# Kernel optimization log

Hardware: AMD Instinct MI355X
Metric: run time of the kernel (lower is better)

The kernel has to match this reference:

```python
import jax, jax.numpy as jnp
import numpy as np

K, D, S, H = 8, 2, 1, 12  # kernel_size, dilation, stride, h_size


def setup_inputs() -> dict:
    key = jax.random.key(0)
    k1, k2 = jax.random.split(key)
    x = jax.random.normal(k1, (32, 2048, 64), dtype=jnp.float32)
    A = jax.random.normal(k2, (64, H, H), dtype=jnp.float32) * 0.1
    return {"x": x, "A": A}


def reference(x, A):
    B, T, C = x.shape
    pad = (K + (K - 1) * (D - 1) - 1) // 2  # = 7
    # replicate padding along time
    xp = jnp.pad(x, ((0, 0), (pad, pad), (0, 0)), mode='edge')  # (B, Tp, C)
    Tp = xp.shape[1]
    seg = (Tp - (K - 1) * D - 1) // S + 1
    # dilated unfold: gather overlapping windows along time
    idx = jnp.arange(seg)[:, None] * S + jnp.arange(K)[None, :] * D  # (seg, K)
    win = xp[:, idx, :]                       # (B, seg, K, C)
    w = win.reshape(B * seg, K, C)            # (N, K, C)
    # path increments within each window
    dx = w[:, 1:, :] - w[:, :-1, :]           # (N, K-1, C)
    # skew-symmetric (so(n)) parametrisation of the Lie-algebra map
    Ask = A - jnp.swapaxes(A, -1, -2)         # (C, H, H)
    M = jnp.einsum('nkc,chw->nkhw', dx, Ask)  # (N, K-1, H, H)
    # matrix exponential of each increment's Lie-algebra element
    E = jax.vmap(jax.scipy.linalg.expm)(M.reshape(-1, H, H)).reshape(M.shape)
    # sequential development: z_{t+1} = z_t @ exp(M_t), z_0 = I
    z0 = jnp.broadcast_to(jnp.eye(H, dtype=x.dtype), (B * seg, H, H))

    def step(z, e):
        return jnp.matmul(z, e), None

    zT, _ = jax.lax.scan(step, z0, jnp.swapaxes(E, 0, 1))  # scan over K-1 steps
    dev = zT.reshape(B, seg, H * H)
    sp = w[:, 0, :].reshape(B, seg, C)        # start point of each partition
    return jnp.concatenate([dev, sp], axis=-1)  # (B, seg, H*H + C)
```

## Files before the change

### kernel.cpp

```cpp
#include <hip/hip_runtime.h>

#define B_ 32
#define T_ 2048
#define C_ 64
#define NP_ 2060
#define MSTRIDE 144
#define LSTRIDE 148
#define W3_ 96
#define NE3_ 110

typedef short short8_t __attribute__((ext_vector_type(8)));
typedef float f32x4 __attribute__((ext_vector_type(4)));

__device__ __forceinline__ unsigned short f2bf(float f) {
  unsigned u = __float_as_uint(f);
  return (unsigned short)((u + 0x7FFFu + ((u >> 16) & 1u)) >> 16);
}
__device__ __forceinline__ float bf2f(unsigned short s) {
  return __uint_as_float(((unsigned)s) << 16);
}

__global__ __launch_bounds__(256) void k1_mfma(const float* __restrict__ x,
                                               const float* __restrict__ A,
                                               float* __restrict__ M) {
  __shared__ unsigned int askw[9216];
  const int b = blockIdx.y;
  const int p0 = blockIdx.x * 64;
  const int tid = threadIdx.x;
  const float sc = 1.0f / 32.0f;

  for (int P = tid; P < 4608; P += 256) {
    const int j2 = P & 3;
    const int col = (P >> 2) & 15;
    const int koct = (P >> 6) & 3;
    const int rest = P >> 8;
    const int tile = rest % 9;
    const int ks = rest / 9;
    const int e = tile * 16 + col;
    const int h = e / 12, w = e - h * 12;
    const int c0 = ks * 32 + koct * 8 + j2 * 2;
    const float v0 = (A[c0 * 144 + e] - A[c0 * 144 + w * 12 + h]) * sc;
    const float v1 = (A[(c0 + 1) * 144 + e] - A[(c0 + 1) * 144 + w * 12 + h]) * sc;
    const unsigned short h0 = f2bf(v0), h1 = f2bf(v1);
    const unsigned short l0 = f2bf(v0 - bf2f(h0)), l1 = f2bf(v1 - bf2f(h1));
    const int widx = (((ks * 9 + tile) * 4 + koct) * 16 + col) * 4 + j2;
    askw[widx] = ((unsigned)h1 << 16) | h0;
    askw[4608 + widx] = ((unsigned)l1 << 16) | l0;
  }
  __syncthreads();

  const int wv = tid >> 6;
  const int lane = tid & 63;
  const int mrow = lane & 15;
  const int koct = lane >> 4;
  const int p = p0 + wv * 16 + mrow;
  const int i1 = min(max(p - 7, 0), T_ - 1);
  const int i2 = min(max(p - 5, 0), T_ - 1);
  const float* xb = x + (size_t)b * T_ * C_;

  short8_t ah[2], al[2];
#pragma unroll
  for (int ks = 0; ks < 2; ++ks) {
    const int c0 = ks * 32 + koct * 8;
    const float4 u1a = *(const float4*)(xb + (size_t)i1 * C_ + c0);
    const float4 u1b = *(const float4*)(xb + (size_t)i1 * C_ + c0 + 4);
    const float4 u2a = *(const float4*)(xb + (size_t)i2 * C_ + c0);
    const float4 u2b = *(const float4*)(xb + (size_t)i2 * C_ + c0 + 4);
    float d[8];
    d[0] = u2a.x - u1a.x; d[1] = u2a.y - u1a.y;
    d[2] = u2a.z - u1a.z; d[3] = u2a.w - u1a.w;
    d[4] = u2b.x - u1b.x; d[5] = u2b.y - u1b.y;
    d[6] = u2b.z - u1b.z; d[7] = u2b.w - u1b.w;
#pragma unroll
    for (int j = 0; j < 8; ++j) {
      const unsigned short hs = f2bf(d[j]);
      ah[ks][j] = (short)hs;
      al[ks][j] = (short)f2bf(d[j] - bf2f(hs));
    }
  }

  float* Mb = M + (size_t)b * NP_ * MSTRIDE;
  const int dcol = lane & 15;
  const int pbase = p0 + wv * 16 + (lane >> 4) * 4;
  const char* lds = (const char*)askw;
#pragma unroll
  for (int tile = 0; tile < 9; ++tile) {
    f32x4 acc = {0.f, 0.f, 0.f, 0.f};
#pragma unroll
    for (int ks = 0; ks < 2; ++ks) {
      const int fb = (((ks * 9 + tile) * 4 + koct) * 16 + dcol) * 16;
      const short8_t bh = *(const short8_t*)(lds + fb);
      const short8_t bl = *(const short8_t*)(lds + 18432 + fb);
      acc = __builtin_amdgcn_mfma_f32_16x16x32_bf16(ah[ks], bh, acc, 0, 0, 0);
      acc = __builtin_amdgcn_mfma_f32_16x16x32_bf16(ah[ks], bl, acc, 0, 0, 0);
      acc = __builtin_amdgcn_mfma_f32_16x16x32_bf16(al[ks], bh, acc, 0, 0, 0);
    }
#pragma unroll
    for (int reg = 0; reg < 4; ++reg) {
      const int pr = pbase + reg;
      if (pr < NP_) Mb[(size_t)pr * MSTRIDE + tile * 16 + dcol] = acc[reg];
    }
  }
}

template <int Q>
__device__ __forceinline__ float qb(float v) {
  return __int_as_float(
      __builtin_amdgcn_mov_dpp(__float_as_int(v), Q * 0x55, 0xf, 0xf, true));
}

template <bool ACC>
__device__ __forceinline__ void qmm_t(const float a[3][12], const float b[3][12],
                                      float c[3][12]) {
  if (!ACC) {
#pragma unroll
    for (int i = 0; i < 3; ++i)
#pragma unroll
      for (int j = 0; j < 12; ++j) c[i][j] = 0.f;
  }
#define QMM_K(OWNER, E)                                                  \
  {                                                                      \
    float bk[12];                                                        \
    _Pragma("unroll")                                                    \
    for (int j = 0; j < 12; ++j) bk[j] = qb<OWNER>(b[E][j]);             \
    _Pragma("unroll")                                                    \
    for (int i = 0; i < 3; ++i) {                                        \
      const float av = a[i][3 * OWNER + E];                              \
      _Pragma("unroll")                                                  \
      for (int j = 0; j < 12; ++j) c[i][j] = fmaf(av, bk[j], c[i][j]);   \
    }                                                                    \
  }
  QMM_K(0, 0) QMM_K(0, 1) QMM_K(0, 2)
  QMM_K(1, 0) QMM_K(1, 1) QMM_K(1, 2)
  QMM_K(2, 0) QMM_K(2, 1) QMM_K(2, 2)
  QMM_K(3, 0) QMM_K(3, 1) QMM_K(3, 2)
#undef QMM_K
}
__device__ __forceinline__ void qmm(const float a[3][12], const float b[3][12],
                                    float c[3][12]) { qmm_t<false>(a, b, c); }
__device__ __forceinline__ void qmma(const float a[3][12], const float b[3][12],
                                     float c[3][12]) { qmm_t<true>(a, b, c); }

__global__ __launch_bounds__(256) void k2_expm(float* __restrict__ M) {
  const int gq = (blockIdx.x * 256 + threadIdx.x) >> 2;
  const int r = threadIdx.x & 3;
  float* gp = M + (size_t)gq * MSTRIDE + 36 * r;

  float a[3][12], t2[3][12], t3[3][12];
#pragma unroll
  for (int i = 0; i < 3; ++i)
#pragma unroll
    for (int q4 = 0; q4 < 3; ++q4) {
      float4 v = *(const float4*)(gp + i * 12 + q4 * 4);
      a[i][q4 * 4 + 0] = v.x;
      a[i][q4 * 4 + 1] = v.y;
      a[i][q4 * 4 + 2] = v.z;
      a[i][q4 * 4 + 3] = v.w;
    }

  qmm(a, a, t2);
  qmm(t2, a, t3);
#pragma unroll
  for (int i = 0; i < 3; ++i)
#pragma unroll
    for (int j = 0; j < 12; ++j) {
      const float av = a[i][j], t2v = t2[i][j], t3v = t3[i][j];
      t2[i][j] = av + t2v * 0.5f + t3v * (1.0f / 6.0f) +
                 ((j == 3 * r + i) ? 1.0f : 0.0f);
      a[i][j] = av * (1.0f / 24.0f) + t2v * (1.0f / 120.0f) +
                t3v * (1.0f / 720.0f);
    }
  qmma(t3, a, t2);

  qmm(t2, t2, t3);
  qmm(t3, t3, t2);
  qmm(t2, t2, t3);
  qmm(t3, t3, t2);
  qmm(t2, t2, t3);

#pragma unroll
  for (int i = 0; i < 3; ++i)
#pragma unroll
    for (int q4 = 0; q4 < 3; ++q4)
      *(float4*)(gp + i * 12 + q4 * 4) =
          make_float4(t3[i][q4 * 4 + 0], t3[i][q4 * 4 + 1],
                      t3[i][q4 * 4 + 2], t3[i][q4 * 4 + 3]);
}

__global__ __launch_bounds__(256) void k3_pair(const float* __restrict__ E,
                                               const float* __restrict__ x,
                                               float* __restrict__ out) {
  __shared__ float eb[NE3_][LSTRIDE];
  const int b = blockIdx.y;
  const int t0 = blockIdx.x * W3_;
  const float* src = E + (size_t)b * NP_ * MSTRIDE;
  for (int i = threadIdx.x; i < NE3_ * 36; i += 256) {
    const int m = i / 36, q = i - m * 36;
    const int p = min(t0 + m, NP_ - 1);
    *(float4*)(&eb[m][q * 4]) = *(const float4*)(src + (size_t)p * MSTRIDE + q * 4);
  }
  __syncthreads();

  const int r = threadIdx.x & 3;
  const int pr = threadIdx.x >> 2;
  if (pr >= 48) return;
  const int par = pr & 1, jj = pr >> 1;
  const int tloc = 4 * jj + par;
  const int t1 = t0 + tloc;

#define LOADB(DST, IDX)                                                  \
  {                                                                      \
    _Pragma("unroll")                                                    \
    for (int i = 0; i < 3; ++i) {                                        \
      const float* ep = &eb[(IDX)][(3 * r + i) * 12];                    \
      float4 v0 = *(const float4*)(ep + 0);                              \
      float4 v1 = *(const float4*)(ep + 4);                              \
      float4 v2 = *(const float4*)(ep + 8);                              \
      DST[i][0] = v0.x; DST[i][1] = v0.y; DST[i][2]  = v0.z; DST[i][3]  = v0.w; \
      DST[i][4] = v1.x; DST[i][5] = v1.y; DST[i][6]  = v1.z; DST[i][7]  = v1.w; \
      DST[i][8] = v2.x; DST[i][9] = v2.y; DST[i][10] = v2.z; DST[i][11] = v2.w; \
    }                                                                    \
  }

#define STOREZ(SRCZ, TW)                                                 \
  {                                                                      \
    const size_t obase = ((size_t)b * T_ + (TW)) * 208;                  \
    _Pragma("unroll")                                                    \
    for (int i = 0; i < 3; ++i) {                                        \
      const int row = 3 * r + i;                                         \
      *(float4*)(out + obase + row * 12 + 0) =                           \
          make_float4(SRCZ[i][0], SRCZ[i][1], SRCZ[i][2],  SRCZ[i][3]);  \
      *(float4*)(out + obase + row * 12 + 4) =                           \
          make_float4(SRCZ[i][4], SRCZ[i][5], SRCZ[i][6],  SRCZ[i][7]);  \
      *(float4*)(out + obase + row * 12 + 8) =                           \
          make_float4(SRCZ[i][8], SRCZ[i][9], SRCZ[i][10], SRCZ[i][11]); \
    }                                                                    \
    const int xi = min(max((TW) - 7, 0), T_ - 1);                        \
    const float* xr = x + ((size_t)b * T_ + xi) * C_ + 16 * r;           \
    _Pragma("unroll")                                                    \
    for (int qd = 0; qd < 4; ++qd) {                                     \
      *(float4*)(out + obase + 144 + 16 * r + qd * 4) =                  \
          *(const float4*)(xr + qd * 4);                                 \
    }                                                                    \
  }

  float rr[3][12], cc[3][12], bb[3][12];
  LOADB(rr, tloc + 2);
  LOADB(bb, tloc + 4);  qmm(rr, bb, cc);
  LOADB(bb, tloc + 6);  qmm(cc, bb, rr);
  LOADB(bb, tloc + 8);  qmm(rr, bb, cc);
  LOADB(bb, tloc + 10); qmm(cc, bb, rr);
  LOADB(bb, tloc + 12); qmm(rr, bb, cc);

  LOADB(bb, tloc);      qmm(bb, cc, rr);
  if (t1 < T_) STOREZ(rr, t1);
  LOADB(bb, tloc + 14); qmm(cc, bb, rr);
  if (t1 + 2 < T_) STOREZ(rr, t1 + 2);
#undef LOADB
#undef STOREZ
}

extern "C" void kernel_launch(void* const* d_in, const int* in_sizes, int n_in,
                              void* d_out, int out_size, void* d_ws, size_t ws_size,
                              hipStream_t stream) {
  (void)in_sizes; (void)n_in; (void)out_size;
  const float* x = (const float*)d_in[0];
  const float* A = (const float*)d_in[1];
  float* out = (float*)d_out;
  float* M = (float*)d_ws;

  const size_t need = (size_t)B_ * NP_ * MSTRIDE * sizeof(float);
  if (ws_size < need) return;

  k1_mfma<<<dim3(33, B_), 256, 0, stream>>>(x, A, M);
  k2_expm<<<dim3((B_ * NP_ * 4) / 256), 256, 0, stream>>>(M);
  k3_pair<<<dim3((T_ + W3_ - 1) / W3_, B_), 256, 0, stream>>>(M, x, out);
}
```

Baseline: 122.0 us.

## Drop one expm squaring step and read k3 matrices straight from global memory

The expm scaling factor is reduced from 1/32 to 1/16, so the squaring phase needs one fewer 12x12 matrix multiply per element. This trades a little Taylor accuracy for less compute in the exponential kernel. The pair-product kernel no longer stages E matrices through shared memory. Each thread now loads directly from global/L2 with all 256 threads active over a 128-step tile, removing the shared-memory fill, the barrier and the idle threads, at the cost of redundant global reads.

```diff
diff --git a/kernel.cpp b/kernel.cpp
--- a/kernel.cpp
+++ b/kernel.cpp
@@ -5,9 +5,6 @@
 #define C_ 64
 #define NP_ 2060
 #define MSTRIDE 144
-#define LSTRIDE 148
-#define W3_ 96
-#define NE3_ 110
 
 typedef short short8_t __attribute__((ext_vector_type(8)));
 typedef float f32x4 __attribute__((ext_vector_type(4)));
@@ -27,7 +24,7 @@
   const int b = blockIdx.y;
   const int p0 = blockIdx.x * 64;
   const int tid = threadIdx.x;
-  const float sc = 1.0f / 32.0f;
+  const float sc = 1.0f / 16.0f;
 
   for (int P = tid; P < 4608; P += 256) {
     const int j2 = P & 3;
@@ -176,46 +173,37 @@
   qmm(t3, t3, t2);
   qmm(t2, t2, t3);
   qmm(t3, t3, t2);
-  qmm(t2, t2, t3);
 
 #pragma unroll
   for (int i = 0; i < 3; ++i)
 #pragma unroll
     for (int q4 = 0; q4 < 3; ++q4)
       *(float4*)(gp + i * 12 + q4 * 4) =
-          make_float4(t3[i][q4 * 4 + 0], t3[i][q4 * 4 + 1],
-                      t3[i][q4 * 4 + 2], t3[i][q4 * 4 + 3]);
+          make_float4(t2[i][q4 * 4 + 0], t2[i][q4 * 4 + 1],
+                      t2[i][q4 * 4 + 2], t2[i][q4 * 4 + 3]);
 }
 
 __global__ __launch_bounds__(256) void k3_pair(const float* __restrict__ E,
                                                const float* __restrict__ x,
                                                float* __restrict__ out) {
-  __shared__ float eb[NE3_][LSTRIDE];
   const int b = blockIdx.y;
-  const int t0 = blockIdx.x * W3_;
-  const float* src = E + (size_t)b * NP_ * MSTRIDE;
-  for (int i = threadIdx.x; i < NE3_ * 36; i += 256) {
-    const int m = i / 36, q = i - m * 36;
-    const int p = min(t0 + m, NP_ - 1);
-    *(float4*)(&eb[m][q * 4]) = *(const float4*)(src + (size_t)p * MSTRIDE + q * 4);
-  }
-  __syncthreads();
+  const int t0 = blockIdx.x * 128;
+  const float* Eb = E + (size_t)b * NP_ * MSTRIDE;
 
   const int r = threadIdx.x & 3;
-  const int pr = threadIdx.x >> 2;
-  if (pr >= 48) return;
-  const int par = pr & 1, jj = pr >> 1;
+  const int q = threadIdx.x >> 2;
+  const int par = q & 1, jj = q >> 1;
   const int tloc = 4 * jj + par;
   const int t1 = t0 + tloc;
 
-#define LOADB(DST, IDX)                                                  \
+#define LOADB_G(DST, P)                                                  \
   {                                                                      \
+    const float* ep = Eb + (size_t)(P) * MSTRIDE + (3 * r) * 12;         \
     _Pragma("unroll")                                                    \
     for (int i = 0; i < 3; ++i) {                                        \
-      const float* ep = &eb[(IDX)][(3 * r + i) * 12];                    \
-      float4 v0 = *(const float4*)(ep + 0);                              \
-      float4 v1 = *(const float4*)(ep + 4);                              \
-      float4 v2 = *(const float4*)(ep + 8);                              \
+      float4 v0 = *(const float4*)(ep + i * 12 + 0);                     \
+      float4 v1 = *(const float4*)(ep + i * 12 + 4);                     \
+      float4 v2 = *(const float4*)(ep + i * 12 + 8);                     \
       DST[i][0] = v0.x; DST[i][1] = v0.y; DST[i][2]  = v0.z; DST[i][3]  = v0.w; \
       DST[i][4] = v1.x; DST[i][5] = v1.y; DST[i][6]  = v1.z; DST[i][7]  = v1.w; \
       DST[i][8] = v2.x; DST[i][9] = v2.y; DST[i][10] = v2.z; DST[i][11] = v2.w; \
@@ -245,18 +233,18 @@
   }
 
   float rr[3][12], cc[3][12], bb[3][12];
-  LOADB(rr, tloc + 2);
-  LOADB(bb, tloc + 4);  qmm(rr, bb, cc);
-  LOADB(bb, tloc + 6);  qmm(cc, bb, rr);
-  LOADB(bb, tloc + 8);  qmm(rr, bb, cc);
-  LOADB(bb, tloc + 10); qmm(cc, bb, rr);
-  LOADB(bb, tloc + 12); qmm(rr, bb, cc);
-
-  LOADB(bb, tloc);      qmm(bb, cc, rr);
-  if (t1 < T_) STOREZ(rr, t1);
-  LOADB(bb, tloc + 14); qmm(cc, bb, rr);
-  if (t1 + 2 < T_) STOREZ(rr, t1 + 2);
-#undef LOADB
+  LOADB_G(rr, t1 + 2);
+  LOADB_G(bb, t1 + 4);  qmm(rr, bb, cc);
+  LOADB_G(bb, t1 + 6);  qmm(cc, bb, rr);
+  LOADB_G(bb, t1 + 8);  qmm(rr, bb, cc);
+  LOADB_G(bb, t1 + 10); qmm(cc, bb, rr);
+  LOADB_G(bb, t1 + 12); qmm(rr, bb, cc);
+
+  LOADB_G(bb, t1);      qmm(bb, cc, rr);
+  STOREZ(rr, t1);
+  LOADB_G(bb, t1 + 14); qmm(cc, bb, rr);
+  STOREZ(rr, t1 + 2);
+#undef LOADB_G
 #undef STOREZ
 }
 
@@ -274,5 +262,5 @@
 
   k1_mfma<<<dim3(33, B_), 256, 0, stream>>>(x, A, M);
   k2_expm<<<dim3((B_ * NP_ * 4) / 256), 256, 0, stream>>>(M);
-  k3_pair<<<dim3((T_ + W3_ - 1) / W3_, B_), 256, 0, stream>>>(M, x, out);
-}
+  k3_pair<<<dim3(T_ / 128, B_), 256, 0, stream>>>(M, x, out);
+}
```

New measurement: 104.4 us. -14.4%, faster.
